# Kernel tuning notes

Measured on AMD Instinct MI355X. Metric: run time of the kernel, lower is better.

Reference implementation:

```python
import jax, jax.numpy as jnp
import numpy as np

B, L, D, H = 1, 2048, 512, 8
HD = D // H  # head dim = 64
EPS = 1e-05
NFFT = 4096  # nearest power of two >= 2*L-1 (causal full conv length)


def _l2norm(t):
    # F.normalize(p=2, dim=-1, eps=EPS)
    return t / jnp.maximum(jnp.linalg.norm(t, axis=-1, keepdims=True), EPS)


def setup_inputs() -> dict:
    key = jax.random.key(0)
    ks = jax.random.split(key, 10)
    s = 0.02
    return {
        "x": jax.random.normal(ks[0], (B, L, D), jnp.float32),
        "spectral_basis": jax.random.normal(ks[1], (L, D), jnp.float32),
        "wq_w": s * jax.random.normal(ks[2], (D, D), jnp.float32),
        "wq_b": jnp.zeros((D,), jnp.float32),
        "wk_w": s * jax.random.normal(ks[3], (D, D), jnp.float32),
        "wk_b": jnp.zeros((D,), jnp.float32),
        "wv_w": s * jax.random.normal(ks[4], (D, D), jnp.float32),
        "wv_b": jnp.zeros((D,), jnp.float32),
        "wo_w": s * jax.random.normal(ks[5], (D, D), jnp.float32),
        "wo_b": jnp.zeros((D,), jnp.float32),
        "td_w": s * jax.random.normal(ks[6], (D, D), jnp.float32),
        "td_b": jnp.zeros((D,), jnp.float32),
        "wgz_w": s * jax.random.normal(ks[7], (1, HD * HD), jnp.float32),
        "wgz_b": jnp.zeros((1,), jnp.float32),
        "kv_norm_scale": jnp.ones((1, 1, 1, HD, HD), jnp.float32),
        "qk_norm_scale": jnp.ones((1, H, 1), jnp.float32) * (1.0 / float(np.sqrt(HD))),
    }


def reference(x, spectral_basis, wq_w, wq_b, wk_w, wk_b, wv_w, wv_b, wo_w, wo_b,
              td_w, td_b, wgz_w, wgz_b, kv_norm_scale, qk_norm_scale):
    Bx, Lx, Dx = x.shape
    # qkv projections -> [B, H, L, h]
    q = (x @ wq_w.T + wq_b).reshape(Bx, Lx, H, HD).transpose(0, 2, 1, 3)
    k = (x @ wk_w.T + wk_b).reshape(Bx, Lx, H, HD).transpose(0, 2, 1, 3)
    v = (x @ wv_w.T + wv_b).reshape(Bx, Lx, H, HD).transpose(0, 2, 1, 3)
    # sim / s / n scan states are computed in the original but do not feed the output
    k_norm = _l2norm(k)
    v_norm = _l2norm(v)
    # spectral filters (tensordot path): [L, D] -> per-head [H, L, h]
    filters = (spectral_basis @ td_w.T + td_b).reshape(Lx, H, HD).transpose(1, 0, 2)
    Ff = jnp.fft.rfft(filters, n=NFFT, axis=1)  # [H, nf, h]

    def causal_conv(u):  # u: [B, H, L, h], per-head per-channel causal FFT conv
        return jnp.fft.irfft(jnp.fft.rfft(u, n=NFFT, axis=2) * Ff[None], n=NFFT, axis=2)[:, :, :Lx]

    k_f = causal_conv(k_norm)
    v_f = causal_conv(v_norm)
    # outer-product KV state per position: [B, H, L, h, h]
    Z = jnp.einsum('bhld,bhle->bhlde', v_f, k_f) * kv_norm_scale
    # gating: Linear(h*h, 1), relu^2 + eps
    logits = Z.reshape(Bx, H, Lx, HD * HD) @ wgz_w.T + wgz_b  # [B, H, L, 1]
    gates = (jax.nn.relu(logits) ** 2 + EPS)[..., None]  # [B, H, L, 1, 1]
    # the combine_fn adds Z and g, so the associative scan over L is a cumsum
    Z_scan = jnp.cumsum(gates * Z, axis=2)
    g_scan = jnp.cumsum(gates, axis=2)
    state = Z_scan / jnp.maximum(g_scan, EPS)  # [B, H, L, h, h]
    sp = _l2norm(jnp.einsum('bhld,bhlde->bhle', q, state))
    return sp.transpose(0, 2, 1, 3).reshape(Bx, Lx, Dx) @ wo_w.T + wo_b
```

## Files before the change

kernel.cpp:

```cpp
#include <hip/hip_runtime.h>
#include <hip/hip_bf16.h>
#include <hip/hip_fp16.h>

#define L_SEQ 2048
#define D_MODEL 512
#define NH 8
#define HD 64
#define EPSF 1e-5f

#define UPAD 2560
#define UOFF 256
#define XLEN 2112
#define XPAD 2120

#define GST 72

typedef __attribute__((ext_vector_type(8))) short short8;
typedef __attribute__((ext_vector_type(8))) _Float16 half8;
typedef __attribute__((ext_vector_type(4))) _Float16 half4v;
typedef __attribute__((ext_vector_type(4))) float f32x4;

__device__ inline short8 cvt8v(const float* __restrict__ p) {
  float4 f0 = *(const float4*)p;
  float4 f1 = *(const float4*)(p + 4);
  short8 r;
  union { __hip_bfloat16 h; short s; } u;
  u.h = __float2bfloat16(f0.x); r[0] = u.s;
  u.h = __float2bfloat16(f0.y); r[1] = u.s;
  u.h = __float2bfloat16(f0.z); r[2] = u.s;
  u.h = __float2bfloat16(f0.w); r[3] = u.s;
  u.h = __float2bfloat16(f1.x); r[4] = u.s;
  u.h = __float2bfloat16(f1.y); r[5] = u.s;
  u.h = __float2bfloat16(f1.z); r[6] = u.s;
  u.h = __float2bfloat16(f1.w); r[7] = u.s;
  return r;
}

__global__ __launch_bounds__(256) void prep_kernel(const float* __restrict__ x,
    const float* __restrict__ sb, const float* __restrict__ wq, const float* __restrict__ wk,
    const float* __restrict__ wv, const float* __restrict__ td, const float* __restrict__ wo,
    __hip_bfloat16* __restrict__ xb, __hip_bfloat16* __restrict__ sbb,
    __hip_bfloat16* __restrict__ wqb, __hip_bfloat16* __restrict__ wkb,
    __hip_bfloat16* __restrict__ wvb, __hip_bfloat16* __restrict__ tdb,
    __hip_bfloat16* __restrict__ wob,
    _Float16* __restrict__ ku16, _Float16* __restrict__ vu16)
{
  int i = blockIdx.x * 256 + threadIdx.x;
  if (i < 425984) {
    size_t base = (size_t)i * 8;
    const float* s;
    __hip_bfloat16* d;
    size_t r;
    if (base < 1048576) { s = x; d = xb; r = base; }
    else if (base < 2097152) { s = sb; d = sbb; r = base - 1048576; }
    else {
      size_t j = base - 2097152;
      int w = (int)(j >> 18);
      r = j & 262143;
      s = (w == 0) ? wq : (w == 1) ? wk : (w == 2) ? wv : (w == 3) ? td : wo;
      d = (w == 0) ? wqb : (w == 1) ? wkb : (w == 2) ? wvb : (w == 3) ? tdb : wob;
    }
    *(short8*)((short*)d + r) = cvt8v(s + r);
  } else if (i < 491520) {
    int t = i - 425984;
    int arr = t >> 15;
    int rem = t & 32767;
    int row = rem >> 6;
    int cc = rem & 63;
    int col = (cc < 32) ? cc * 8 : 2304 + (cc - 32) * 8;
    _Float16* base = arr ? vu16 : ku16;
    *(int4*)(base + (size_t)row * UPAD + col) = int4{0, 0, 0, 0};
  }
}

__global__ __launch_bounds__(256) void gemm4_kernel(
    const __hip_bfloat16* __restrict__ xb, const __hip_bfloat16* __restrict__ sbb,
    const __hip_bfloat16* __restrict__ wqb, const __hip_bfloat16* __restrict__ wkb,
    const __hip_bfloat16* __restrict__ wvb, const __hip_bfloat16* __restrict__ tdb,
    const float* __restrict__ bq, const float* __restrict__ bk,
    const float* __restrict__ bv, const float* __restrict__ btd,
    float* __restrict__ qout, float* __restrict__ fT,
    _Float16* __restrict__ ku16, _Float16* __restrict__ vu16)
{
  __shared__ __align__(16) short lds_s[2][2][64 * GST];
  int z = blockIdx.z;
  const __hip_bfloat16* A = (z == 3) ? sbb : xb;
  const __hip_bfloat16* W = (z == 0) ? wqb : (z == 1) ? wkb : (z == 2) ? wvb : tdb;
  const float* bias = (z == 0) ? bq : (z == 1) ? bk : (z == 2) ? bv : btd;
  const int M = L_SEQ, N = D_MODEL, K = D_MODEL;
  int tid = threadIdx.x;
  int lane = tid & 63;
  int wave = tid >> 6;
  int m_base = blockIdx.x * 64;
  int n_base = blockIdx.y * 64;
  int m0 = m_base + wave * 16;
  int n0 = n_base;
  int lrow = lane & 15, quad = lane >> 4;

  int r0 = tid >> 3, o0 = (tid & 7) * 8;
  int r1 = (tid + 256) >> 3, o1 = (tid & 7) * 8;
  const short* Ag0 = (const short*)A + (size_t)(m_base + r0) * K + o0;
  const short* Ag1 = (const short*)A + (size_t)(m_base + r1) * K + o1;
  const short* Wg0 = (const short*)W + (size_t)(n_base + r0) * K + o0;
  const short* Wg1 = (const short*)W + (size_t)(n_base + r1) * K + o1;
  int la0 = r0 * GST + o0;
  int la1 = r1 * GST + o1;

  f32x4 acc[4] = {};
  short8 ra0 = *(const short8*)(Ag0);
  short8 ra1 = *(const short8*)(Ag1);
  short8 rw0 = *(const short8*)(Wg0);
  short8 rw1 = *(const short8*)(Wg1);
#pragma unroll
  for (int t = 0; t < 8; ++t) {
    const int buf = t & 1;
    *(short8*)(&lds_s[buf][0][la0]) = ra0;
    *(short8*)(&lds_s[buf][0][la1]) = ra1;
    *(short8*)(&lds_s[buf][1][la0]) = rw0;
    *(short8*)(&lds_s[buf][1][la1]) = rw1;
    __syncthreads();
    if (t < 7) {
      ra0 = *(const short8*)(Ag0 + (t + 1) * 64);
      ra1 = *(const short8*)(Ag1 + (t + 1) * 64);
      rw0 = *(const short8*)(Wg0 + (t + 1) * 64);
      rw1 = *(const short8*)(Wg1 + (t + 1) * 64);
    }
    const short* As = lds_s[buf][0];
    const short* Ws = lds_s[buf][1];
#pragma unroll
    for (int kk = 0; kk < 2; ++kk) {
      short8 a = *(const short8*)(As + (wave * 16 + lrow) * GST + kk * 32 + quad * 8);
#pragma unroll
      for (int j = 0; j < 4; ++j) {
        short8 b = *(const short8*)(Ws + (j * 16 + lrow) * GST + kk * 32 + quad * 8);
        acc[j] = __builtin_amdgcn_mfma_f32_16x16x32_bf16(a, b, acc[j], 0, 0, 0);
      }
    }
  }
  float bw[4];
#pragma unroll
  for (int j = 0; j < 4; ++j) bw[j] = bias[n0 + j * 16 + lrow];
  if (z == 0) {
#pragma unroll
    for (int j = 0; j < 4; ++j)
#pragma unroll
      for (int r = 0; r < 4; ++r)
        qout[(size_t)(m0 + quad * 4 + r) * N + n0 + j * 16 + lrow] = acc[j][r] + bw[j];
  } else if (z == 3) {
#pragma unroll
    for (int j = 0; j < 4; ++j) {
      float4 ov = {acc[j][0] + bw[j], acc[j][1] + bw[j], acc[j][2] + bw[j], acc[j][3] + bw[j]};
      *(float4*)(fT + (size_t)(n0 + j * 16 + lrow) * M + m0 + quad * 4) = ov;
    }
  } else {
    float val[4][4];
#pragma unroll
    for (int j = 0; j < 4; ++j)
#pragma unroll
      for (int r = 0; r < 4; ++r) val[j][r] = acc[j][r] + bw[j];
    float pr[4];
#pragma unroll
    for (int r = 0; r < 4; ++r)
      pr[r] = val[0][r] * val[0][r] + val[1][r] * val[1][r] +
              val[2][r] * val[2][r] + val[3][r] * val[3][r];
#pragma unroll
    for (int off = 1; off < 16; off <<= 1)
#pragma unroll
      for (int r = 0; r < 4; ++r)
        pr[r] += __shfl_xor(pr[r], off, 64);
    _Float16* u16 = (z == 1) ? ku16 : vu16;
#pragma unroll
    for (int r = 0; r < 4; ++r) {
      float inv = 1.f / fmaxf(sqrtf(pr[r]), EPSF);
#pragma unroll
      for (int j = 0; j < 4; ++j) val[j][r] *= inv;
    }
#pragma unroll
    for (int j = 0; j < 4; ++j) {
      half4v pk = {(_Float16)val[j][0], (_Float16)val[j][1],
                   (_Float16)val[j][2], (_Float16)val[j][3]};
      *(half4v*)(u16 + (size_t)(n0 + j * 16 + lrow) * UPAD + UOFF + m0 + quad * 4) = pk;
    }
  }
}

__global__ __launch_bounds__(256) void conv_kernel(
    const _Float16* __restrict__ ku16, const _Float16* __restrict__ vu16,
    const float* __restrict__ fT, float* __restrict__ oK, float* __restrict__ oV)
{
  __shared__ _Float16 lds_f[8 * XPAD];
  int c = blockIdx.x;
  int tid = threadIdx.x;
  const float* Fc = fT + (size_t)c * L_SEQ;
#pragma unroll
  for (int s = 0; s < 2; ++s) {
    int idx = tid + s * 256;
    int p = idx >> 6, m = idx & 63;
    int xx = (m < 16 - p) ? m : 2048 + m;
    lds_f[p * XPAD + xx] = (_Float16)0.f;
  }
#pragma unroll
  for (int it = 0; it < 2; ++it) {
    int j0 = it * 1024 + tid * 4;
    float4 f = *(const float4*)(Fc + j0);
    _Float16 h4[4] = {(_Float16)f.x, (_Float16)f.y, (_Float16)f.z, (_Float16)f.w};
#pragma unroll
    for (int e = 0; e < 4; ++e) {
      int xbase = 2063 - (j0 + e);
#pragma unroll
      for (int p = 0; p < 8; ++p)
        lds_f[p * XPAD + (xbase - p)] = h4[e];
    }
  }
  __syncthreads();

  int wave = tid >> 6, lane = tid & 63;
  int pair = wave;
  int l0_lo = 256 * pair;
  int l0_hi = 1792 - l0_lo;
  int mn = lane & 15, quad = lane >> 4;

  const _Float16* puk = ku16 + (size_t)c * UPAD + 16 * mn + 8 * quad;
  const _Float16* puv = vu16 + (size_t)c * UPAD + 16 * mn + 8 * quad;

  int j0c = 2063 - mn;
  int p8 = j0c & 7;
  int xb0 = (j0c - p8) + 8 * quad;
  const _Float16* pf_hi = lds_f + p8 * XPAD + (xb0 - (l0_hi + 256));
  const _Float16* pf_lo = lds_f + p8 * XPAD + (xb0 - (l0_lo + 256));

  int steps_lo = pair * 8 + 9;
  int steps_hi = 65 - pair * 8;
  f32x4 ak_hi = {}, ak_lo = {}, av_hi = {}, av_lo = {};
  half8 bk = *(const half8*)puk;
  half8 bv = *(const half8*)puv;
  half8 fh = *(const half8*)pf_hi;
  half8 fl = *(const half8*)pf_lo;
#pragma unroll 2
  for (int i = 0; i < steps_lo; ++i) {
    puk += 32; puv += 32; pf_hi += 32; pf_lo += 32;
    half8 bk_n = *(const half8*)puk;
    half8 bv_n = *(const half8*)puv;
    half8 fh_n = *(const half8*)pf_hi;
    half8 fl_n = *(const half8*)pf_lo;
    ak_hi = __builtin_amdgcn_mfma_f32_16x16x32_f16(fh, bk, ak_hi, 0, 0, 0);
    av_hi = __builtin_amdgcn_mfma_f32_16x16x32_f16(fh, bv, av_hi, 0, 0, 0);
    ak_lo = __builtin_amdgcn_mfma_f32_16x16x32_f16(fl, bk, ak_lo, 0, 0, 0);
    av_lo = __builtin_amdgcn_mfma_f32_16x16x32_f16(fl, bv, av_lo, 0, 0, 0);
    bk = bk_n; bv = bv_n; fh = fh_n; fl = fl_n;
  }
#pragma unroll 2
  for (int i = steps_lo; i < steps_hi; ++i) {
    puk += 32; puv += 32; pf_hi += 32;
    half8 bk_n = *(const half8*)puk;
    half8 bv_n = *(const half8*)puv;
    half8 fh_n = *(const half8*)pf_hi;
    ak_hi = __builtin_amdgcn_mfma_f32_16x16x32_f16(fh, bk, ak_hi, 0, 0, 0);
    av_hi = __builtin_amdgcn_mfma_f32_16x16x32_f16(fh, bv, av_hi, 0, 0, 0);
    bk = bk_n; bv = bv_n; fh = fh_n;
  }
  size_t ob = (size_t)c * L_SEQ + 16 * mn + 4 * quad;
  *(float4*)(oK + ob + l0_hi) = float4{ak_hi[0], ak_hi[1], ak_hi[2], ak_hi[3]};
  *(float4*)(oK + ob + l0_lo) = float4{ak_lo[0], ak_lo[1], ak_lo[2], ak_lo[3]};
  *(float4*)(oV + ob + l0_hi) = float4{av_hi[0], av_hi[1], av_hi[2], av_hi[3]};
  *(float4*)(oV + ob + l0_lo) = float4{av_lo[0], av_lo[1], av_lo[2], av_lo[3]};
}

__global__ __launch_bounds__(256) void gatepart_kernel(const float* __restrict__ kf,
    const float* __restrict__ vf, const float* __restrict__ wgz_w,
    const float* __restrict__ wgz_b, const float* __restrict__ kvs,
    float* __restrict__ g, float* __restrict__ A, float* __restrict__ gsum)
{
  __shared__ float MT[64][68];
  __shared__ float kb[64][68];
  __shared__ float kbT[64][68];
  __shared__ float vb[64][68];
  __shared__ float yb[64][68];
  __shared__ float part[4][64];
  __shared__ float gl[64];
  int h = blockIdx.y, ch = blockIdx.x;
  int t0 = ch * 64, tid = threadIdx.x;
#pragma unroll
  for (int k = 0; k < 4; ++k) {
    int e = tid + k * 256;
    int a = e >> 4, b4 = (e & 15) * 4;
    float4 wv = *(const float4*)(wgz_w + a * 64 + b4);
    float4 sv = *(const float4*)(kvs + a * 64 + b4);
    MT[b4 + 0][a] = wv.x * sv.x;
    MT[b4 + 1][a] = wv.y * sv.y;
    MT[b4 + 2][a] = wv.z * sv.z;
    MT[b4 + 3][a] = wv.w * sv.w;
    float4 kv = *(const float4*)(kf + (size_t)(h * 64 + a) * L_SEQ + t0 + b4);
    *(float4*)(&kb[a][b4]) = kv;
    kbT[b4 + 0][a] = kv.x;
    kbT[b4 + 1][a] = kv.y;
    kbT[b4 + 2][a] = kv.z;
    kbT[b4 + 3][a] = kv.w;
    float4 vv = *(const float4*)(vf + (size_t)(h * 64 + a) * L_SEQ + t0 + b4);
    *(float4*)(&vb[a][b4]) = vv;
  }
  __syncthreads();
  int lg = tid & 15, dg = tid >> 4;
  {
    float acc[4][4] = {};
    for (int e = 0; e < 64; ++e) {
      float4 mv4 = *(const float4*)(&MT[e][dg * 4]);
      float4 kv4 = *(const float4*)(&kb[e][lg * 4]);
      float mvv[4] = {mv4.x, mv4.y, mv4.z, mv4.w};
      float kvv[4] = {kv4.x, kv4.y, kv4.z, kv4.w};
#pragma unroll
      for (int r = 0; r < 4; ++r)
#pragma unroll
        for (int j = 0; j < 4; ++j)
          acc[r][j] = fmaf(mvv[r], kvv[j], acc[r][j]);
    }
#pragma unroll
    for (int r = 0; r < 4; ++r)
#pragma unroll
      for (int j = 0; j < 4; ++j)
        yb[dg * 4 + r][lg * 4 + j] = acc[r][j];
  }
  __syncthreads();
  {
    int l = tid & 63, p = tid >> 6;
    float s = 0.f;
#pragma unroll
    for (int dd = 0; dd < 16; ++dd)
      s = fmaf(yb[p * 16 + dd][l], vb[p * 16 + dd][l], s);
    part[p][l] = s;
  }
  __syncthreads();
  if (tid < 64) {
    float logit = part[0][tid] + part[1][tid] + part[2][tid] + part[3][tid] + wgz_b[0];
    float rl = fmaxf(logit, 0.f);
    float gv = rl * rl + EPSF;
    g[h * L_SEQ + t0 + tid] = gv;
    gl[tid] = gv;
  }
  __syncthreads();
  if (tid < 64) {
    float s = gl[tid];
#pragma unroll
    for (int off = 1; off < 64; off <<= 1) s += __shfl_xor(s, off, 64);
    if (tid == 0) gsum[h * 32 + ch] = s;
  }
  int eg = tid & 15, dg2 = tid >> 4;
  float acc[4][4] = {};
  for (int t = 0; t < 64; ++t) {
    float gt = gl[t];
    float4 k4 = *(const float4*)(&kbT[t][eg * 4]);
    float kv4[4] = {k4.x * gt, k4.y * gt, k4.z * gt, k4.w * gt};
    float vv4[4];
#pragma unroll
    for (int r = 0; r < 4; ++r) vv4[r] = vb[dg2 * 4 + r][t];
#pragma unroll
    for (int r = 0; r < 4; ++r)
#pragma unroll
      for (int j = 0; j < 4; ++j)
        acc[r][j] = fmaf(vv4[r], kv4[j], acc[r][j]);
  }
  float* Ap = A + ((size_t)(h * 32 + ch)) * 4096;
#pragma unroll
  for (int r = 0; r < 4; ++r)
#pragma unroll
    for (int j = 0; j < 4; ++j)
      Ap[(dg2 * 4 + r) * 64 + eg * 4 + j] = acc[r][j];
}

__global__ void prefix_kernel(float* __restrict__ A, float* __restrict__ gsum)
{
  int flat = blockIdx.x * 256 + threadIdx.x;
  int h = flat >> 12, de = flat & 4095;
  size_t base = (size_t)h * 32 * 4096 + de;
  float v[32];
#pragma unroll
  for (int c = 0; c < 32; ++c) v[c] = A[base + (size_t)c * 4096];
  float run = 0.f;
#pragma unroll
  for (int c = 0; c < 32; ++c) {
    A[base + (size_t)c * 4096] = run;
    run += v[c];
  }
  if (flat < 8) {
    float t[32];
#pragma unroll
    for (int c = 0; c < 32; ++c) t[c] = gsum[flat * 32 + c];
    float r = 0.f;
#pragma unroll
    for (int c = 0; c < 32; ++c) { gsum[flat * 32 + c] = r; r += t[c]; }
  }
}

__global__ __launch_bounds__(256) void attn_kernel(const float* __restrict__ q,
    const float* __restrict__ kf, const float* __restrict__ vf, const float* __restrict__ g,
    const float* __restrict__ Sprev, const float* __restrict__ Gprev,
    __hip_bfloat16* __restrict__ sp)
{
  __shared__ float qT[64][68];
  __shared__ float SW[64][69];
  __shared__ float vb[64][68];
  __shared__ float kb[64][69];
  __shared__ float gl[64], Gs[64], rsq[64];
  int h = blockIdx.y, ch = blockIdx.x;
  int t0 = ch * 64, tid = threadIdx.x;
  const float* Sp = Sprev + ((size_t)(h * 32 + ch)) * 4096;
#pragma unroll
  for (int k = 0; k < 4; ++k) {
    int e = tid + k * 256;
    int a = e >> 4, b4 = (e & 15) * 4;
    float4 qv = *(const float4*)(q + (size_t)(t0 + a) * D_MODEL + h * 64 + b4);
    qT[b4 + 0][a] = qv.x;
    qT[b4 + 1][a] = qv.y;
    qT[b4 + 2][a] = qv.z;
    qT[b4 + 3][a] = qv.w;
    float4 sv = *(const float4*)(Sp + a * 64 + b4);
    SW[a][b4 + 0] = sv.x;
    SW[a][b4 + 1] = sv.y;
    SW[a][b4 + 2] = sv.z;
    SW[a][b4 + 3] = sv.w;
    float4 vv = *(const float4*)(vf + (size_t)(h * 64 + a) * L_SEQ + t0 + b4);
    *(float4*)(&vb[a][b4]) = vv;
    float4 kv = *(const float4*)(kf + (size_t)(h * 64 + a) * L_SEQ + t0 + b4);
    kb[a][b4 + 0] = kv.x;
    kb[a][b4 + 1] = kv.y;
    kb[a][b4 + 2] = kv.z;
    kb[a][b4 + 3] = kv.w;
  }
  if (tid < 64) { gl[tid] = g[h * L_SEQ + t0 + tid]; rsq[tid] = 0.f; }
  __syncthreads();
  if (tid < 64) {
    float val = gl[tid];
#pragma unroll
    for (int off = 1; off < 64; off <<= 1) {
      float o = __shfl_up(val, (unsigned)off, 64);
      if (tid >= off) val += o;
    }
    Gs[tid] = fmaxf(Gprev[h * 32 + ch] + val, EPSF);
  }
  int lg = tid & 15, eg = tid >> 4;
  float acc[4][4] = {};
  float sc[4][4] = {};
  for (int d = 0; d < 64; ++d) {
    float4 q4 = *(const float4*)(&qT[d][lg * 4]);
    float qv[4] = {q4.x, q4.y, q4.z, q4.w};
    float sv[4];
#pragma unroll
    for (int j = 0; j < 4; ++j) sv[j] = SW[d][eg * 4 + j];
    float4 v4 = *(const float4*)(&vb[d][eg * 4]);
    float vv[4] = {v4.x, v4.y, v4.z, v4.w};
#pragma unroll
    for (int r = 0; r < 4; ++r)
#pragma unroll
      for (int j = 0; j < 4; ++j) {
        acc[r][j] = fmaf(qv[r], sv[j], acc[r][j]);
        sc[r][j] = fmaf(qv[r], vv[j], sc[r][j]);
      }
  }
  __syncthreads();
#pragma unroll
  for (int r = 0; r < 4; ++r)
#pragma unroll
    for (int m = 0; m < 4; ++m) {
      int ll = lg * 4 + r, tt = eg * 4 + m;
      SW[ll][tt] = (tt <= ll) ? sc[r][m] * gl[tt] : 0.f;
    }
  __syncthreads();
  for (int t = 0; t < 64; ++t) {
    float wv4[4], kv4[4];
#pragma unroll
    for (int r = 0; r < 4; ++r) wv4[r] = SW[lg * 4 + r][t];
#pragma unroll
    for (int j = 0; j < 4; ++j) kv4[j] = kb[eg * 4 + j][t];
#pragma unroll
    for (int r = 0; r < 4; ++r)
#pragma unroll
      for (int j = 0; j < 4; ++j)
        acc[r][j] = fmaf(wv4[r], kv4[j], acc[r][j]);
  }
  float val[4][4];
  int egw = (tid >> 4) & 3;
#pragma unroll
  for (int r = 0; r < 4; ++r) {
    float gi = 1.f / Gs[lg * 4 + r];
    float pr = 0.f;
#pragma unroll
    for (int j = 0; j < 4; ++j) { float v = acc[r][j] * gi; val[r][j] = v; pr = fmaf(v, v, pr); }
    pr += __shfl_xor(pr, 16, 64);
    pr += __shfl_xor(pr, 32, 64);
    if (egw == 0) atomicAdd(&rsq[lg * 4 + r], pr);
  }
  __syncthreads();
#pragma unroll
  for (int r = 0; r < 4; ++r) {
    float inv = 1.f / fmaxf(sqrtf(rsq[lg * 4 + r]), EPSF);
    union { ushort4 u; __hip_bfloat16 hh[4]; } pk;
#pragma unroll
    for (int j = 0; j < 4; ++j) pk.hh[j] = __float2bfloat16(val[r][j] * inv);
    *(ushort4*)(sp + (size_t)(t0 + lg * 4 + r) * D_MODEL + h * 64 + eg * 4) = pk.u;
  }
}

__global__ __launch_bounds__(256) void gemm_out_kernel(const __hip_bfloat16* __restrict__ A,
    const __hip_bfloat16* __restrict__ W, const float* __restrict__ bias,
    float* __restrict__ O)
{
  __shared__ __align__(16) short lds_s[2][2][64 * GST];
  const int N = D_MODEL, K = D_MODEL;
  int tid = threadIdx.x;
  int lane = tid & 63;
  int wave = tid >> 6;
  int m_base = blockIdx.x * 64;
  int n_base = blockIdx.y * 64;
  int m0 = m_base + wave * 16;
  int n0 = n_base;
  int lrow = lane & 15, quad = lane >> 4;

  int r0 = tid >> 3, o0 = (tid & 7) * 8;
  int r1 = (tid + 256) >> 3, o1 = (tid & 7) * 8;
  const short* Ag0 = (const short*)A + (size_t)(m_base + r0) * K + o0;
  const short* Ag1 = (const short*)A + (size_t)(m_base + r1) * K + o1;
  const short* Wg0 = (const short*)W + (size_t)(n_base + r0) * K + o0;
  const short* Wg1 = (const short*)W + (size_t)(n_base + r1) * K + o1;
  int la0 = r0 * GST + o0;
  int la1 = r1 * GST + o1;

  f32x4 acc[4] = {};
  short8 ra0 = *(const short8*)(Ag0);
  short8 ra1 = *(const short8*)(Ag1);
  short8 rw0 = *(const short8*)(Wg0);
  short8 rw1 = *(const short8*)(Wg1);
#pragma unroll
  for (int t = 0; t < 8; ++t) {
    const int buf = t & 1;
    *(short8*)(&lds_s[buf][0][la0]) = ra0;
    *(short8*)(&lds_s[buf][0][la1]) = ra1;
    *(short8*)(&lds_s[buf][1][la0]) = rw0;
    *(short8*)(&lds_s[buf][1][la1]) = rw1;
    __syncthreads();
    if (t < 7) {
      ra0 = *(const short8*)(Ag0 + (t + 1) * 64);
      ra1 = *(const short8*)(Ag1 + (t + 1) * 64);
      rw0 = *(const short8*)(Wg0 + (t + 1) * 64);
      rw1 = *(const short8*)(Wg1 + (t + 1) * 64);
    }
    const short* As = lds_s[buf][0];
    const short* Ws = lds_s[buf][1];
#pragma unroll
    for (int kk = 0; kk < 2; ++kk) {
      short8 a = *(const short8*)(As + (wave * 16 + lrow) * GST + kk * 32 + quad * 8);
#pragma unroll
      for (int j = 0; j < 4; ++j) {
        short8 b = *(const short8*)(Ws + (j * 16 + lrow) * GST + kk * 32 + quad * 8);
        acc[j] = __builtin_amdgcn_mfma_f32_16x16x32_bf16(a, b, acc[j], 0, 0, 0);
      }
    }
  }
#pragma unroll
  for (int j = 0; j < 4; ++j) {
    int n = n0 + j * 16 + lrow;
    float bv = bias[n];
#pragma unroll
    for (int r = 0; r < 4; ++r)
      O[(size_t)(m0 + quad * 4 + r) * N + n] = acc[j][r] + bv;
  }
}

extern "C" void kernel_launch(void* const* d_in, const int* in_sizes, int n_in,
                              void* d_out, int out_size, void* d_ws, size_t ws_size,
                              hipStream_t stream) {
  const float* x = (const float*)d_in[0];
  const float* sb = (const float*)d_in[1];
  const float* wq_w = (const float*)d_in[2];
  const float* wq_b = (const float*)d_in[3];
  const float* wk_w = (const float*)d_in[4];
  const float* wk_b = (const float*)d_in[5];
  const float* wv_w = (const float*)d_in[6];
  const float* wv_b = (const float*)d_in[7];
  const float* wo_w = (const float*)d_in[8];
  const float* wo_b = (const float*)d_in[9];
  const float* td_w = (const float*)d_in[10];
  const float* td_b = (const float*)d_in[11];
  const float* wgz_w = (const float*)d_in[12];
  const float* wgz_b = (const float*)d_in[13];
  const float* kvs = (const float*)d_in[14];
  float* out = (float*)d_out;

  char* ws = (char*)d_ws;
  size_t off = 0;
  auto alloc = [&](size_t bytes) -> void* {
    void* p = ws + off;
    off += (bytes + 255) & ~(size_t)255;
    return p;
  };
  __hip_bfloat16* xb  = (__hip_bfloat16*)alloc((size_t)L_SEQ * D_MODEL * 2);
  __hip_bfloat16* sbb = (__hip_bfloat16*)alloc((size_t)L_SEQ * D_MODEL * 2);
  __hip_bfloat16* wqb = (__hip_bfloat16*)alloc((size_t)D_MODEL * D_MODEL * 2);
  __hip_bfloat16* wkb = (__hip_bfloat16*)alloc((size_t)D_MODEL * D_MODEL * 2);
  __hip_bfloat16* wvb = (__hip_bfloat16*)alloc((size_t)D_MODEL * D_MODEL * 2);
  __hip_bfloat16* tdb = (__hip_bfloat16*)alloc((size_t)D_MODEL * D_MODEL * 2);
  __hip_bfloat16* wob = (__hip_bfloat16*)alloc((size_t)D_MODEL * D_MODEL * 2);
  __hip_bfloat16* spb = (__hip_bfloat16*)alloc((size_t)L_SEQ * D_MODEL * 2);
  _Float16* ku16 = (_Float16*)alloc((size_t)D_MODEL * UPAD * 2);
  _Float16* vu16 = (_Float16*)alloc((size_t)D_MODEL * UPAD * 2);
  float* qbuf  = (float*)alloc((size_t)L_SEQ * D_MODEL * 4);
  float* fT    = (float*)alloc((size_t)D_MODEL * L_SEQ * 4);
  float* kfT   = (float*)alloc((size_t)D_MODEL * L_SEQ * 4);
  float* vfT   = (float*)alloc((size_t)D_MODEL * L_SEQ * 4);
  float* gbuf  = (float*)alloc((size_t)NH * L_SEQ * 4);
  float* gsum  = (float*)alloc((size_t)NH * 32 * 4);
  float* Abuf  = (float*)alloc((size_t)NH * 32 * 4096 * 4);

  prep_kernel<<<1920, 256, 0, stream>>>(x, sb, wq_w, wk_w, wv_w, td_w, wo_w,
                                        xb, sbb, wqb, wkb, wvb, tdb, wob,
                                        ku16, vu16);
  gemm4_kernel<<<dim3(L_SEQ / 64, D_MODEL / 64, 4), 256, 0, stream>>>(
      xb, sbb, wqb, wkb, wvb, tdb, wq_b, wk_b, wv_b, td_b, qbuf, fT,
      ku16, vu16);
  conv_kernel<<<512, 256, 0, stream>>>(ku16, vu16, fT, kfT, vfT);
  gatepart_kernel<<<dim3(32, 8), 256, 0, stream>>>(kfT, vfT, wgz_w, wgz_b, kvs, gbuf, Abuf, gsum);
  prefix_kernel<<<128, 256, 0, stream>>>(Abuf, gsum);
  attn_kernel<<<dim3(32, 8), 256, 0, stream>>>(qbuf, kfT, vfT, gbuf, Abuf, gsum, spb);
  gemm_out_kernel<<<dim3(L_SEQ / 64, D_MODEL / 64), 256, 0, stream>>>(spb, wob, wo_b, out);
}
```

Baseline: 153.8 us.

## Fuse conv, gating, prefix, attention and output GEMM into cooperative megakernel

Replaces five separate kernel launches (conv, gatepart, prefix, attn, gemm_out) with one cooperative kernel of 256 blocks that uses grid.sync between phases. The conv phase now runs with 256 blocks, each doing two channels instead of one. The goal is to remove launch gaps and the drain and refill between kernels. The risk is lower parallelism in some phases, the cost of the grid barriers, and a larger LDS footprint that could limit occupancy. The original five-kernel path is kept as a fallback when cooperative launch fails.

```diff
diff --git a/kernel.cpp b/kernel.cpp
--- a/kernel.cpp
+++ b/kernel.cpp
@@ -1,6 +1,9 @@
 #include <hip/hip_runtime.h>
 #include <hip/hip_bf16.h>
 #include <hip/hip_fp16.h>
+#include <hip/hip_cooperative_groups.h>
+
+namespace cg = cooperative_groups;
 
 #define L_SEQ 2048
 #define D_MODEL 512
@@ -562,6 +565,392 @@
 #pragma unroll
     for (int r = 0; r < 4; ++r)
       O[(size_t)(m0 + quad * 4 + r) * N + n] = acc[j][r] + bv;
+  }
+}
+
+__global__ __launch_bounds__(256) void mega_kernel(
+    const _Float16* __restrict__ ku16, const _Float16* __restrict__ vu16,
+    const float* __restrict__ fT, float* __restrict__ kfT, float* __restrict__ vfT,
+    const float* __restrict__ wgz_w, const float* __restrict__ wgz_b,
+    const float* __restrict__ kvs, float* __restrict__ g, float* __restrict__ Abuf,
+    float* __restrict__ gsum, const float* __restrict__ q,
+    __hip_bfloat16* __restrict__ sp, const __hip_bfloat16* __restrict__ wo,
+    const float* __restrict__ wo_bias, float* __restrict__ out)
+{
+  cg::grid_group grid = cg::this_grid();
+  __shared__ __align__(16) char smem[88448];
+  int tid = threadIdx.x;
+  int bx = blockIdx.x, by = blockIdx.y;
+  int flat = by * 32 + bx;
+
+  {
+    _Float16* lds_f = (_Float16*)smem;
+    int wave = tid >> 6, lane = tid & 63;
+    int pair = wave;
+    int l0_lo = 256 * pair;
+    int l0_hi = 1792 - l0_lo;
+    int mn = lane & 15, quad = lane >> 4;
+    int j0c = 2063 - mn;
+    int p8 = j0c & 7;
+    int xb0 = (j0c - p8) + 8 * quad;
+    int steps_lo = pair * 8 + 9;
+    int steps_hi = 65 - pair * 8;
+#pragma unroll 1
+    for (int ci = 0; ci < 2; ++ci) {
+      int c = flat * 2 + ci;
+      const float* Fc = fT + (size_t)c * L_SEQ;
+      __syncthreads();
+#pragma unroll
+      for (int s = 0; s < 2; ++s) {
+        int idx = tid + s * 256;
+        int p = idx >> 6, m = idx & 63;
+        int xx = (m < 16 - p) ? m : 2048 + m;
+        lds_f[p * XPAD + xx] = (_Float16)0.f;
+      }
+#pragma unroll
+      for (int it = 0; it < 2; ++it) {
+        int j0 = it * 1024 + tid * 4;
+        float4 f = *(const float4*)(Fc + j0);
+        _Float16 h4[4] = {(_Float16)f.x, (_Float16)f.y, (_Float16)f.z, (_Float16)f.w};
+#pragma unroll
+        for (int e = 0; e < 4; ++e) {
+          int xbase = 2063 - (j0 + e);
+#pragma unroll
+          for (int p = 0; p < 8; ++p)
+            lds_f[p * XPAD + (xbase - p)] = h4[e];
+        }
+      }
+      __syncthreads();
+      const _Float16* puk = ku16 + (size_t)c * UPAD + 16 * mn + 8 * quad;
+      const _Float16* puv = vu16 + (size_t)c * UPAD + 16 * mn + 8 * quad;
+      const _Float16* pf_hi = lds_f + p8 * XPAD + (xb0 - (l0_hi + 256));
+      const _Float16* pf_lo = lds_f + p8 * XPAD + (xb0 - (l0_lo + 256));
+      f32x4 ak_hi = {}, ak_lo = {}, av_hi = {}, av_lo = {};
+      half8 bk = *(const half8*)puk;
+      half8 bv = *(const half8*)puv;
+      half8 fh = *(const half8*)pf_hi;
+      half8 fl = *(const half8*)pf_lo;
+#pragma unroll 2
+      for (int i = 0; i < steps_lo; ++i) {
+        puk += 32; puv += 32; pf_hi += 32; pf_lo += 32;
+        half8 bk_n = *(const half8*)puk;
+        half8 bv_n = *(const half8*)puv;
+        half8 fh_n = *(const half8*)pf_hi;
+        half8 fl_n = *(const half8*)pf_lo;
+        ak_hi = __builtin_amdgcn_mfma_f32_16x16x32_f16(fh, bk, ak_hi, 0, 0, 0);
+        av_hi = __builtin_amdgcn_mfma_f32_16x16x32_f16(fh, bv, av_hi, 0, 0, 0);
+        ak_lo = __builtin_amdgcn_mfma_f32_16x16x32_f16(fl, bk, ak_lo, 0, 0, 0);
+        av_lo = __builtin_amdgcn_mfma_f32_16x16x32_f16(fl, bv, av_lo, 0, 0, 0);
+        bk = bk_n; bv = bv_n; fh = fh_n; fl = fl_n;
+      }
+#pragma unroll 2
+      for (int i = steps_lo; i < steps_hi; ++i) {
+        puk += 32; puv += 32; pf_hi += 32;
+        half8 bk_n = *(const half8*)puk;
+        half8 bv_n = *(const half8*)puv;
+        half8 fh_n = *(const half8*)pf_hi;
+        ak_hi = __builtin_amdgcn_mfma_f32_16x16x32_f16(fh, bk, ak_hi, 0, 0, 0);
+        av_hi = __builtin_amdgcn_mfma_f32_16x16x32_f16(fh, bv, av_hi, 0, 0, 0);
+        bk = bk_n; bv = bv_n; fh = fh_n;
+      }
+      size_t ob = (size_t)c * L_SEQ + 16 * mn + 4 * quad;
+      *(float4*)(kfT + ob + l0_hi) = float4{ak_hi[0], ak_hi[1], ak_hi[2], ak_hi[3]};
+      *(float4*)(kfT + ob + l0_lo) = float4{ak_lo[0], ak_lo[1], ak_lo[2], ak_lo[3]};
+      *(float4*)(vfT + ob + l0_hi) = float4{av_hi[0], av_hi[1], av_hi[2], av_hi[3]};
+      *(float4*)(vfT + ob + l0_lo) = float4{av_lo[0], av_lo[1], av_lo[2], av_lo[3]};
+    }
+  }
+  grid.sync();
+
+  {
+    float (*MT)[68]   = (float (*)[68])(smem);
+    float (*kb)[68]   = (float (*)[68])(smem + 17408);
+    float (*kbT)[68]  = (float (*)[68])(smem + 34816);
+    float (*vb)[68]   = (float (*)[68])(smem + 52224);
+    float (*yb)[68]   = (float (*)[68])(smem + 69632);
+    float (*part)[64] = (float (*)[64])(smem + 87040);
+    float* gl         = (float*)(smem + 88064);
+    int h = by, ch = bx;
+    int t0 = ch * 64;
+#pragma unroll
+    for (int k = 0; k < 4; ++k) {
+      int e = tid + k * 256;
+      int a = e >> 4, b4 = (e & 15) * 4;
+      float4 wv = *(const float4*)(wgz_w + a * 64 + b4);
+      float4 sv = *(const float4*)(kvs + a * 64 + b4);
+      MT[b4 + 0][a] = wv.x * sv.x;
+      MT[b4 + 1][a] = wv.y * sv.y;
+      MT[b4 + 2][a] = wv.z * sv.z;
+      MT[b4 + 3][a] = wv.w * sv.w;
+      float4 kv = *(const float4*)(kfT + (size_t)(h * 64 + a) * L_SEQ + t0 + b4);
+      *(float4*)(&kb[a][b4]) = kv;
+      kbT[b4 + 0][a] = kv.x;
+      kbT[b4 + 1][a] = kv.y;
+      kbT[b4 + 2][a] = kv.z;
+      kbT[b4 + 3][a] = kv.w;
+      float4 vv = *(const float4*)(vfT + (size_t)(h * 64 + a) * L_SEQ + t0 + b4);
+      *(float4*)(&vb[a][b4]) = vv;
+    }
+    __syncthreads();
+    int lg = tid & 15, dg = tid >> 4;
+    {
+      float acc[4][4] = {};
+      for (int e = 0; e < 64; ++e) {
+        float4 mv4 = *(const float4*)(&MT[e][dg * 4]);
+        float4 kv4 = *(const float4*)(&kb[e][lg * 4]);
+        float mvv[4] = {mv4.x, mv4.y, mv4.z, mv4.w};
+        float kvv[4] = {kv4.x, kv4.y, kv4.z, kv4.w};
+#pragma unroll
+        for (int r = 0; r < 4; ++r)
+#pragma unroll
+          for (int j = 0; j < 4; ++j)
+            acc[r][j] = fmaf(mvv[r], kvv[j], acc[r][j]);
+      }
+#pragma unroll
+      for (int r = 0; r < 4; ++r)
+#pragma unroll
+        for (int j = 0; j < 4; ++j)
+          yb[dg * 4 + r][lg * 4 + j] = acc[r][j];
+    }
+    __syncthreads();
+    {
+      int l = tid & 63, p = tid >> 6;
+      float s = 0.f;
+#pragma unroll
+      for (int dd = 0; dd < 16; ++dd)
+        s = fmaf(yb[p * 16 + dd][l], vb[p * 16 + dd][l], s);
+      part[p][l] = s;
+    }
+    __syncthreads();
+    if (tid < 64) {
+      float logit = part[0][tid] + part[1][tid] + part[2][tid] + part[3][tid] + wgz_b[0];
+      float rl = fmaxf(logit, 0.f);
+      float gv = rl * rl + EPSF;
+      g[h * L_SEQ + t0 + tid] = gv;
+      gl[tid] = gv;
+    }
+    __syncthreads();
+    if (tid < 64) {
+      float s = gl[tid];
+#pragma unroll
+      for (int off = 1; off < 64; off <<= 1) s += __shfl_xor(s, off, 64);
+      if (tid == 0) gsum[h * 32 + ch] = s;
+    }
+    int eg = tid & 15, dg2 = tid >> 4;
+    float acc[4][4] = {};
+    for (int t = 0; t < 64; ++t) {
+      float gt = gl[t];
+      float4 k4 = *(const float4*)(&kbT[t][eg * 4]);
+      float kv4[4] = {k4.x * gt, k4.y * gt, k4.z * gt, k4.w * gt};
+      float vv4[4];
+#pragma unroll
+      for (int r = 0; r < 4; ++r) vv4[r] = vb[dg2 * 4 + r][t];
+#pragma unroll
+      for (int r = 0; r < 4; ++r)
+#pragma unroll
+        for (int j = 0; j < 4; ++j)
+          acc[r][j] = fmaf(vv4[r], kv4[j], acc[r][j]);
+    }
+    float* Ap = Abuf + ((size_t)(h * 32 + ch)) * 4096;
+#pragma unroll
+    for (int r = 0; r < 4; ++r)
+#pragma unroll
+      for (int j = 0; j < 4; ++j)
+        Ap[(dg2 * 4 + r) * 64 + eg * 4 + j] = acc[r][j];
+  }
+  grid.sync();
+
+  {
+    int f = flat * 256 + tid;
+    if (f < 32768) {
+      int h = f >> 12, de = f & 4095;
+      size_t base = (size_t)h * 32 * 4096 + de;
+      float v[32];
+#pragma unroll
+      for (int c = 0; c < 32; ++c) v[c] = Abuf[base + (size_t)c * 4096];
+      float run = 0.f;
+#pragma unroll
+      for (int c = 0; c < 32; ++c) {
+        Abuf[base + (size_t)c * 4096] = run;
+        run += v[c];
+      }
+    }
+    if (f < 8) {
+      float t[32];
+#pragma unroll
+      for (int c = 0; c < 32; ++c) t[c] = gsum[f * 32 + c];
+      float r = 0.f;
+#pragma unroll
+      for (int c = 0; c < 32; ++c) { gsum[f * 32 + c] = r; r += t[c]; }
+    }
+  }
+  grid.sync();
+
+  {
+    float (*qT)[68] = (float (*)[68])(smem);
+    float (*SW)[69] = (float (*)[69])(smem + 17408);
+    float (*vb)[68] = (float (*)[68])(smem + 35072);
+    float (*kb)[69] = (float (*)[69])(smem + 52480);
+    float* gl  = (float*)(smem + 70144);
+    float* Gs  = (float*)(smem + 70400);
+    float* rsq = (float*)(smem + 70656);
+    int h = by, ch = bx;
+    int t0 = ch * 64;
+    const float* Sp = Abuf + ((size_t)(h * 32 + ch)) * 4096;
+#pragma unroll
+    for (int k = 0; k < 4; ++k) {
+      int e = tid + k * 256;
+      int a = e >> 4, b4 = (e & 15) * 4;
+      float4 qv = *(const float4*)(q + (size_t)(t0 + a) * D_MODEL + h * 64 + b4);
+      qT[b4 + 0][a] = qv.x;
+      qT[b4 + 1][a] = qv.y;
+      qT[b4 + 2][a] = qv.z;
+      qT[b4 + 3][a] = qv.w;
+      float4 sv = *(const float4*)(Sp + a * 64 + b4);
+      SW[a][b4 + 0] = sv.x;
+      SW[a][b4 + 1] = sv.y;
+      SW[a][b4 + 2] = sv.z;
+      SW[a][b4 + 3] = sv.w;
+      float4 vv = *(const float4*)(vfT + (size_t)(h * 64 + a) * L_SEQ + t0 + b4);
+      *(float4*)(&vb[a][b4]) = vv;
+      float4 kv = *(const float4*)(kfT + (size_t)(h * 64 + a) * L_SEQ + t0 + b4);
+      kb[a][b4 + 0] = kv.x;
+      kb[a][b4 + 1] = kv.y;
+      kb[a][b4 + 2] = kv.z;
+      kb[a][b4 + 3] = kv.w;
+    }
+    if (tid < 64) { gl[tid] = g[h * L_SEQ + t0 + tid]; rsq[tid] = 0.f; }
+    __syncthreads();
+    if (tid < 64) {
+      float val = gl[tid];
+#pragma unroll
+      for (int off = 1; off < 64; off <<= 1) {
+        float o = __shfl_up(val, (unsigned)off, 64);
+        if (tid >= off) val += o;
+      }
+      Gs[tid] = fmaxf(gsum[h * 32 + ch] + val, EPSF);
+    }
+    int lg = tid & 15, eg = tid >> 4;
+    float acc[4][4] = {};
+    float sc[4][4] = {};
+    for (int d = 0; d < 64; ++d) {
+      float4 q4 = *(const float4*)(&qT[d][lg * 4]);
+      float qv[4] = {q4.x, q4.y, q4.z, q4.w};
+      float sv[4];
+#pragma unroll
+      for (int j = 0; j < 4; ++j) sv[j] = SW[d][eg * 4 + j];
+      float4 v4 = *(const float4*)(&vb[d][eg * 4]);
+      float vv[4] = {v4.x, v4.y, v4.z, v4.w};
+#pragma unroll
+      for (int r = 0; r < 4; ++r)
+#pragma unroll
+        for (int j = 0; j < 4; ++j) {
+          acc[r][j] = fmaf(qv[r], sv[j], acc[r][j]);
+          sc[r][j] = fmaf(qv[r], vv[j], sc[r][j]);
+        }
+    }
+    __syncthreads();
+#pragma unroll
+    for (int r = 0; r < 4; ++r)
+#pragma unroll
+      for (int m = 0; m < 4; ++m) {
+        int ll = lg * 4 + r, tt = eg * 4 + m;
+        SW[ll][tt] = (tt <= ll) ? sc[r][m] * gl[tt] : 0.f;
+      }
+    __syncthreads();
+    for (int t = 0; t < 64; ++t) {
+      float wv4[4], kv4[4];
+#pragma unroll
+      for (int r = 0; r < 4; ++r) wv4[r] = SW[lg * 4 + r][t];
+#pragma unroll
+      for (int j = 0; j < 4; ++j) kv4[j] = kb[eg * 4 + j][t];
+#pragma unroll
+      for (int r = 0; r < 4; ++r)
+#pragma unroll
+        for (int j = 0; j < 4; ++j)
+          acc[r][j] = fmaf(wv4[r], kv4[j], acc[r][j]);
+    }
+    float val[4][4];
+    int egw = (tid >> 4) & 3;
+#pragma unroll
+    for (int r = 0; r < 4; ++r) {
+      float gi = 1.f / Gs[lg * 4 + r];
+      float pr = 0.f;
+#pragma unroll
+      for (int j = 0; j < 4; ++j) { float v = acc[r][j] * gi; val[r][j] = v; pr = fmaf(v, v, pr); }
+      pr += __shfl_xor(pr, 16, 64);
+      pr += __shfl_xor(pr, 32, 64);
+      if (egw == 0) atomicAdd(&rsq[lg * 4 + r], pr);
+    }
+    __syncthreads();
+#pragma unroll
+    for (int r = 0; r < 4; ++r) {
+      float inv = 1.f / fmaxf(sqrtf(rsq[lg * 4 + r]), EPSF);
+      union { ushort4 u; __hip_bfloat16 hh[4]; } pk;
+#pragma unroll
+      for (int j = 0; j < 4; ++j) pk.hh[j] = __float2bfloat16(val[r][j] * inv);
+      *(ushort4*)(sp + (size_t)(t0 + lg * 4 + r) * D_MODEL + h * 64 + eg * 4) = pk.u;
+    }
+  }
+  grid.sync();
+
+  {
+    short (*lds_s)[2][64 * GST] = (short (*)[2][64 * GST])smem;
+    const int N = D_MODEL, K = D_MODEL;
+    int lane = tid & 63;
+    int wave = tid >> 6;
+    int m_base = bx * 64;
+    int n_base = by * 64;
+    int m0 = m_base + wave * 16;
+    int n0 = n_base;
+    int lrow = lane & 15, quad = lane >> 4;
+    int r0 = tid >> 3, o0 = (tid & 7) * 8;
+    int r1 = (tid + 256) >> 3, o1 = (tid & 7) * 8;
+    const short* Ag0 = (const short*)sp + (size_t)(m_base + r0) * K + o0;
+    const short* Ag1 = (const short*)sp + (size_t)(m_base + r1) * K + o1;
+    const short* Wg0 = (const short*)wo + (size_t)(n_base + r0) * K + o0;
+    const short* Wg1 = (const short*)wo + (size_t)(n_base + r1) * K + o1;
+    int la0 = r0 * GST + o0;
+    int la1 = r1 * GST + o1;
+    f32x4 acc[4] = {};
+    short8 ra0 = *(const short8*)(Ag0);
+    short8 ra1 = *(const short8*)(Ag1);
+    short8 rw0 = *(const short8*)(Wg0);
+    short8 rw1 = *(const short8*)(Wg1);
+#pragma unroll
+    for (int t = 0; t < 8; ++t) {
+      const int buf = t & 1;
+      *(short8*)(&lds_s[buf][0][la0]) = ra0;
+      *(short8*)(&lds_s[buf][0][la1]) = ra1;
+      *(short8*)(&lds_s[buf][1][la0]) = rw0;
+      *(short8*)(&lds_s[buf][1][la1]) = rw1;
+      __syncthreads();
+      if (t < 7) {
+        ra0 = *(const short8*)(Ag0 + (t + 1) * 64);
+        ra1 = *(const short8*)(Ag1 + (t + 1) * 64);
+        rw0 = *(const short8*)(Wg0 + (t + 1) * 64);
+        rw1 = *(const short8*)(Wg1 + (t + 1) * 64);
+      }
+      const short* As = lds_s[buf][0];
+      const short* Ws = lds_s[buf][1];
+#pragma unroll
+      for (int kk = 0; kk < 2; ++kk) {
+        short8 a = *(const short8*)(As + (wave * 16 + lrow) * GST + kk * 32 + quad * 8);
+#pragma unroll
+        for (int j = 0; j < 4; ++j) {
+          short8 b = *(const short8*)(Ws + (j * 16 + lrow) * GST + kk * 32 + quad * 8);
+          acc[j] = __builtin_amdgcn_mfma_f32_16x16x32_bf16(a, b, acc[j], 0, 0, 0);
+        }
+      }
+    }
+#pragma unroll
+    for (int j = 0; j < 4; ++j) {
+      int n = n0 + j * 16 + lrow;
+      float bv = wo_bias[n];
+#pragma unroll
+      for (int r = 0; r < 4; ++r)
+        out[(size_t)(m0 + quad * 4 + r) * N + n] = acc[j][r] + bv;
+    }
   }
 }
 
@@ -610,15 +999,39 @@
   float* gsum  = (float*)alloc((size_t)NH * 32 * 4);
   float* Abuf  = (float*)alloc((size_t)NH * 32 * 4096 * 4);
 
+  static int coop = -1;
+  if (coop < 0) {
+    int v = 0;
+    int dev = 0;
+    hipGetDevice(&dev);
+    hipDeviceGetAttribute(&v, hipDeviceAttributeCooperativeLaunch, dev);
+    coop = v;
+  }
+
   prep_kernel<<<1920, 256, 0, stream>>>(x, sb, wq_w, wk_w, wv_w, td_w, wo_w,
                                         xb, sbb, wqb, wkb, wvb, tdb, wob,
                                         ku16, vu16);
   gemm4_kernel<<<dim3(L_SEQ / 64, D_MODEL / 64, 4), 256, 0, stream>>>(
       xb, sbb, wqb, wkb, wvb, tdb, wq_b, wk_b, wv_b, td_b, qbuf, fT,
       ku16, vu16);
-  conv_kernel<<<512, 256, 0, stream>>>(ku16, vu16, fT, kfT, vfT);
-  gatepart_kernel<<<dim3(32, 8), 256, 0, stream>>>(kfT, vfT, wgz_w, wgz_b, kvs, gbuf, Abuf, gsum);
-  prefix_kernel<<<128, 256, 0, stream>>>(Abuf, gsum);
-  attn_kernel<<<dim3(32, 8), 256, 0, stream>>>(qbuf, kfT, vfT, gbuf, Abuf, gsum, spb);
-  gemm_out_kernel<<<dim3(L_SEQ / 64, D_MODEL / 64), 256, 0, stream>>>(spb, wob, wo_b, out);
+
+  bool done = false;
+  if (coop) {
+    void* margs[] = {
+      (void*)&ku16, (void*)&vu16, (void*)&fT, (void*)&kfT, (void*)&vfT,
+      (void*)&wgz_w, (void*)&wgz_b, (void*)&kvs, (void*)&gbuf, (void*)&Abuf,
+      (void*)&gsum, (void*)&qbuf, (void*)&spb, (void*)&wob, (void*)&wo_b,
+      (void*)&out};
+    hipError_t e = hipLaunchCooperativeKernel((const void*)mega_kernel,
+                                              dim3(32, 8), dim3(256),
+                                              margs, 0, stream);
+    done = (e == hipSuccess);
+  }
+  if (!done) {
+    conv_kernel<<<512, 256, 0, stream>>>(ku16, vu16, fT, kfT, vfT);
+    gatepart_kernel<<<dim3(32, 8), 256, 0, stream>>>(kfT, vfT, wgz_w, wgz_b, kvs, gbuf, Abuf, gsum);
+    prefix_kernel<<<128, 256, 0, stream>>>(Abuf, gsum);
+    attn_kernel<<<dim3(32, 8), 256, 0, stream>>>(qbuf, kfT, vfT, gbuf, Abuf, gsum, spb);
+    gemm_out_kernel<<<dim3(L_SEQ / 64, D_MODEL / 64), 256, 0, stream>>>(spb, wob, wo_b, out);
+  }
 }
```

Measured after the change: 313.5 us. 2.04x slower.
